# Kernel tuning notes

Hardware: AMD Instinct MI355X
Metric: run time of the kernel (lower is better)

## Reference

```python
import jax, jax.numpy as jnp
import numpy as np

B, N, Q, H = 32, 1024, 64, 768


def setup_inputs() -> dict:
    key = jax.random.key(0)
    k1, k2, k3, k4 = jax.random.split(key, 4)
    return {
        "nodes_compress": jax.random.normal(k1, (B, N, H), dtype=jnp.float32),
        "query_compress": jax.random.normal(k2, (B, Q, H), dtype=jnp.float32),
        "nodes_hidden": jax.random.normal(k3, (B, N, H), dtype=jnp.float32),
        # nn.Linear(3H, 1, bias=False).weight flattened to (3H,)
        "w": jax.random.normal(k4, (3 * H,), dtype=jnp.float32) * (1.0 / np.sqrt(3 * H)),
    }


def reference(nodes_compress, query_compress, nodes_hidden, w):
    h = nodes_compress.shape[-1]
    w_n, w_q, w_nq = w[:h], w[h:2 * h], w[2 * h:]
    # Decomposed trilinear similarity: identical to Linear([n, q, n*q]) -> scalar
    sim = (
        (nodes_compress @ w_n)[:, :, None]          # (B, N, 1)
        + (query_compress @ w_q)[:, None, :]        # (B, 1, Q)
        + jnp.einsum("bnh,bqh,h->bnq", nodes_compress, query_compress, w_nq)
    )                                                # (B, N, Q)
    # nodes -> query attention
    a = jax.nn.softmax(sim, axis=-1)                 # (B, N, Q)
    nodes2query = jnp.einsum("bnq,bqh->bnh", a, query_compress)
    # query -> nodes attention (max over query, softmax over nodes)
    b = jax.nn.softmax(jnp.max(sim, axis=-1), axis=-1)  # (B, N)
    q2n = jnp.einsum("bn,bnh->bh", b, nodes_compress)[:, None, :]  # (B, 1, H)
    q2n = jnp.broadcast_to(q2n, nodes_compress.shape)               # (B, N, H)
    return jnp.concatenate(
        [nodes_compress, nodes2query, nodes_compress * nodes2query, nodes_compress * q2n],
        axis=-1,
    )  # (B, N, 4H)
```

## Files before the change

### kernel.cpp

```cpp
#include <hip/hip_runtime.h>
#include <hip/hip_bf16.h>

#define BB 32
#define NN 1024
#define QQ 64
#define HH 768

typedef __attribute__((ext_vector_type(8))) short short8;
typedef __attribute__((ext_vector_type(4))) float f32x4;

#define GLOAD_LDS16(gp, lp) \
  __builtin_amdgcn_global_load_lds((const __attribute__((address_space(1))) unsigned int*)(gp), \
                                   (__attribute__((address_space(3))) unsigned int*)(lp), 16, 0, 0)

__device__ __forceinline__ unsigned short f2b(float f) {
  unsigned int u = __float_as_uint(f);
  unsigned int r = u + 0x7fffu + ((u >> 16) & 1u);
  return (unsigned short)(r >> 16);
}

__global__ void k_prep(const float* __restrict__ qc, const float* __restrict__ w,
                       unsigned short* __restrict__ qwB, unsigned short* __restrict__ qcT,
                       float* __restrict__ sq) {
  const int bid = blockIdx.x, tid = threadIdx.x;
  if (bid < 768) {
    int gid = bid * 256 + tid;
    int b = gid / 6144, rem = gid % 6144;
    int q = rem / 96, kk = rem % 96;
    int kc = kk >> 4, uu = kk & 15;
    const float* src = qc + ((size_t)(b * 64 + q) * HH + kk * 8);
    float4 g0 = *(const float4*)src, g1 = *(const float4*)(src + 4);
    int h = kk * 8;
    float4 n0 = *(const float4*)(w + h), n1 = *(const float4*)(w + h + 4);
    float4 m0 = *(const float4*)(w + 2 * HH + h), m1 = *(const float4*)(w + 2 * HH + h + 4);
    short8 v;
    v[0] = (short)f2b(g0.x * m0.x + n0.x); v[1] = (short)f2b(g0.y * m0.y + n0.y);
    v[2] = (short)f2b(g0.z * m0.z + n0.z); v[3] = (short)f2b(g0.w * m0.w + n0.w);
    v[4] = (short)f2b(g1.x * m1.x + n1.x); v[5] = (short)f2b(g1.y * m1.y + n1.y);
    v[6] = (short)f2b(g1.z * m1.z + n1.z); v[7] = (short)f2b(g1.w * m1.w + n1.w);
    size_t du = (size_t)(b * 6 + kc) * 1024 + q * 16 + (uu ^ (q & 7));
    *(short8*)((char*)qwB + du * 16) = v;
  } else if (bid < 1536) {
    int gid = (bid - 768) * 256 + tid;
    int b = gid / 6144, p = gid % 6144;
    int hc = p >> 10, pr = p & 1023, r = pr >> 3, x = pr & 7;
    int xu = x ^ (r & 7);
    int h = hc * 128 + r;
    const float* col = qc + ((size_t)(b * 64 + xu * 8) * HH + h);
    short8 v;
#pragma unroll
    for (int j = 0; j < 8; ++j) v[j] = (short)f2b(col[(size_t)j * HH]);
    *(short8*)((char*)qcT + (size_t)gid * 16) = v;
  } else {
    int wid = ((bid - 1536) * 256 + tid) >> 6;
    int l = tid & 63;
    const float* row = qc + (size_t)wid * HH;
    float s = 0.f;
#pragma unroll
    for (int i = 0; i < 12; ++i) s += row[i * 64 + l] * w[HH + i * 64 + l];
#pragma unroll
    for (int m = 1; m < 64; m <<= 1) s += __shfl_xor(s, m);
    if (l == 0) sq[wid] = s;
  }
}

__global__ __launch_bounds__(256) void k_sim(
    const float* __restrict__ nc, const unsigned short* __restrict__ qwB,
    const float* __restrict__ sq, float* __restrict__ partial,
    float* __restrict__ mtse, unsigned short* __restrict__ probs)
{
  __shared__ __align__(16) char bbuf[2][16384];
  __shared__ float rowmF[64];
  __shared__ float wvF[64];

  const int tid = threadIdx.x;
  const int wv_ = tid >> 6, l = tid & 63;
  const int l15 = l & 15, lg = l >> 4;
  const int b = blockIdx.x >> 4, tile = blockIdx.x & 15;
  const int row0 = tile * 64;

  const float* ncB = nc + (size_t)(b * NN + row0) * HH;
  const char* qwb = (const char*)qwB + (size_t)b * 98304;
  const float* aBase = ncB + (wv_ * 16 + l15) * HH + lg * 8;

  {
    const char* gsrc = qwb + wv_ * 4096 + l * 16;
#pragma unroll
    for (int i = 0; i < 4; ++i)
      GLOAD_LDS16(gsrc + i * 1024, &bbuf[0][wv_ * 4096 + i * 1024]);
  }
  float4 fr[2][8];
#pragma unroll
  for (int ks = 0; ks < 4; ++ks) {
    fr[0][ks * 2]     = *(const float4*)(aBase + ks * 32);
    fr[0][ks * 2 + 1] = *(const float4*)(aBase + ks * 32 + 4);
  }

  f32x4 acc[4] = {};
#pragma unroll
  for (int kc = 0; kc < 6; ++kc) {
    short8 af[4];
#pragma unroll
    for (int ks = 0; ks < 4; ++ks) {
      float4 f0 = fr[kc & 1][ks * 2], f1 = fr[kc & 1][ks * 2 + 1];
      short8 v;
      v[0] = (short)f2b(f0.x); v[1] = (short)f2b(f0.y);
      v[2] = (short)f2b(f0.z); v[3] = (short)f2b(f0.w);
      v[4] = (short)f2b(f1.x); v[5] = (short)f2b(f1.y);
      v[6] = (short)f2b(f1.z); v[7] = (short)f2b(f1.w);
      af[ks] = v;
    }
    if (kc < 5) {
#pragma unroll
      for (int ks = 0; ks < 4; ++ks) {
        fr[(kc + 1) & 1][ks * 2]     = *(const float4*)(aBase + (kc + 1) * 128 + ks * 32);
        fr[(kc + 1) & 1][ks * 2 + 1] = *(const float4*)(aBase + (kc + 1) * 128 + ks * 32 + 4);
      }
      const char* gsrc = qwb + (kc + 1) * 16384 + wv_ * 4096 + l * 16;
#pragma unroll
      for (int i = 0; i < 4; ++i)
        GLOAD_LDS16(gsrc + i * 1024, &bbuf[(kc + 1) & 1][wv_ * 4096 + i * 1024]);
      asm volatile("s_waitcnt vmcnt(12)" ::: "memory");
    } else {
      asm volatile("s_waitcnt vmcnt(0)" ::: "memory");
    }
    __builtin_amdgcn_s_barrier();
    __builtin_amdgcn_sched_barrier(0);
#pragma unroll
    for (int ks = 0; ks < 4; ++ks) {
      int kbyte = ks * 64 + lg * 16;
#pragma unroll
      for (int nt = 0; nt < 4; ++nt) {
        int brow = nt * 16 + l15;
        short8 bf = *(short8*)(&bbuf[kc & 1][0] + brow * 256 + (kbyte ^ ((l & 7) << 4)));
        acc[nt] = __builtin_amdgcn_mfma_f32_16x16x32_bf16(af[ks], bf, acc[nt], 0, 0, 0);
      }
    }
    __builtin_amdgcn_sched_barrier(0);
    __builtin_amdgcn_s_barrier();
  }

  unsigned short* pT = probs + (size_t)(b * 16 + tile) * (QQ * QQ);
  float sqv[4];
#pragma unroll
  for (int nt = 0; nt < 4; ++nt) sqv[nt] = sq[b * QQ + nt * 16 + l15];
#pragma unroll
  for (int j = 0; j < 4; ++j) {
    float mm = -1e30f;
#pragma unroll
    for (int nt = 0; nt < 4; ++nt) { acc[nt][j] += sqv[nt]; mm = fmaxf(mm, acc[nt][j]); }
    mm = fmaxf(mm, __shfl_xor(mm, 1));
    mm = fmaxf(mm, __shfl_xor(mm, 2));
    mm = fmaxf(mm, __shfl_xor(mm, 4));
    mm = fmaxf(mm, __shfl_xor(mm, 8));
    float ss = 0.f;
#pragma unroll
    for (int nt = 0; nt < 4; ++nt) { float p = __expf(acc[nt][j] - mm); acc[nt][j] = p; ss += p; }
    ss += __shfl_xor(ss, 1); ss += __shfl_xor(ss, 2);
    ss += __shfl_xor(ss, 4); ss += __shfl_xor(ss, 8);
    float inv = 1.0f / ss;
    int r = wv_ * 16 + lg * 4 + j;
#pragma unroll
    for (int nt = 0; nt < 4; ++nt)
      pT[r * 64 + nt * 16 + l15] = f2b(acc[nt][j] * inv);
    if (l15 == 0) rowmF[r] = mm;
  }
  __syncthreads();

  float m_t = -1e30f;
#pragma unroll
  for (int i = 0; i < 16; ++i) {
    f32x4 v = ((f32x4*)rowmF)[i];
    m_t = fmaxf(m_t, fmaxf(fmaxf(v[0], v[1]), fmaxf(v[2], v[3])));
  }
  if (tid < 64) wvF[tid] = __expf(rowmF[tid] - m_t);
  __syncthreads();
  {
    float sv = wvF[l];
#pragma unroll
    for (int m = 1; m < 64; m <<= 1) sv += __shfl_xor(sv, m);
    if (tid == 0) {
      mtse[(b * 16 + tile) * 2] = m_t;
      mtse[(b * 16 + tile) * 2 + 1] = sv;
    }
  }
  {
    float p0 = 0.f, p1 = 0.f, p2 = 0.f;
    for (int n = 0; n < 64; ++n) {
      float wvv = wvF[n];
      const float* pr = ncB + n * HH + tid;
      p0 += wvv * pr[0]; p1 += wvv * pr[256]; p2 += wvv * pr[512];
    }
    float* pp = partial + (size_t)(b * 16 + tile) * HH + tid;
    pp[0] = p0; pp[256] = p1; pp[512] = p2;
  }
}

__global__ __launch_bounds__(256) void k_out(
    const float* __restrict__ nc, const unsigned short* __restrict__ qcT,
    const unsigned short* __restrict__ probs, const float* __restrict__ partial,
    const float* __restrict__ mtse, float* __restrict__ out)
{
  __shared__ __align__(16) char smem[16384];
  __shared__ float q2nL[128];

  const int tid = threadIdx.x;
  const int wv_ = tid >> 6, l = tid & 63;
  const int l15 = l & 15, lg = l >> 4;
  const int bid = blockIdx.x;
  const int hc = bid % 6;
  const int bt = bid / 6;
  const int b = bt >> 4, tile = bt & 15;
  const int row0 = tile * 64;

  {
    const char* src = (const char*)qcT + ((size_t)(b * 6 + hc) << 14) + wv_ * 4096 + l * 16;
#pragma unroll
    for (int i = 0; i < 4; ++i)
      GLOAD_LDS16(src + i * 1024, &smem[wv_ * 4096 + i * 1024]);
  }

  if (tid < 128) {
    float M = -1e30f, mt[16], se[16];
#pragma unroll
    for (int i = 0; i < 16; ++i) {
      mt[i] = mtse[(b * 16 + i) * 2];
      se[i] = mtse[(b * 16 + i) * 2 + 1];
      M = fmaxf(M, mt[i]);
    }
    float denom = 0.f;
#pragma unroll
    for (int i = 0; i < 16; ++i) { mt[i] = __expf(mt[i] - M); denom += mt[i] * se[i]; }
    float inv = 1.0f / denom;
    float a = 0.f;
#pragma unroll
    for (int i = 0; i < 16; ++i)
      a += mt[i] * partial[(size_t)(b * 16 + i) * HH + hc * 128 + tid];
    q2nL[tid] = a * inv;
  }

  const unsigned short* pT = probs + (size_t)bt * (QQ * QQ);
  short8 a2_0 = *(const short8*)((const char*)pT + (wv_ * 16 + l15) * 128 + lg * 16);
  short8 a2_1 = *(const short8*)((const char*)pT + (wv_ * 16 + l15) * 128 + 64 + lg * 16);

  asm volatile("s_waitcnt vmcnt(0)" ::: "memory");
  __syncthreads();

  const int n = wv_ * 16 + l15;
  const float* ncrow = nc + (size_t)(b * NN + row0 + n) * HH;
  float* orow = out + (size_t)(b * NN + row0 + n) * 3072;

#pragma unroll
  for (int hg = 0; hg < 8; ++hg) {
    f32x4 c2 = {};
#pragma unroll
    for (int ks2 = 0; ks2 < 2; ++ks2) {
      int hrow = hg * 16 + l15;
      int kbyte = ks2 * 64 + lg * 16;
      short8 hf = *(short8*)(&smem[0] + hrow * 128 + (kbyte ^ ((l & 7) << 4)));
      c2 = __builtin_amdgcn_mfma_f32_16x16x32_bf16(hf, ks2 ? a2_1 : a2_0, c2, 0, 0, 0);
    }
    int hl = hg * 16 + lg * 4;
    int hbase = hc * 128 + hl;
    f32x4 ncv = *(const f32x4*)(ncrow + hbase);
    f32x4 qv  = *(const f32x4*)(&q2nL[hl]);
    *(f32x4*)(orow + hbase)          = ncv;
    *(f32x4*)(orow + HH + hbase)     = c2;
    *(f32x4*)(orow + 2 * HH + hbase) = ncv * c2;
    *(f32x4*)(orow + 2304 + hbase)   = ncv * qv;
  }
}

extern "C" void kernel_launch(void* const* d_in, const int* in_sizes, int n_in,
                              void* d_out, int out_size, void* d_ws, size_t ws_size,
                              hipStream_t stream) {
  (void)in_sizes; (void)n_in; (void)out_size; (void)ws_size;
  const float* nc = (const float*)d_in[0];
  const float* qc = (const float*)d_in[1];
  const float* w  = (const float*)d_in[3];
  float* out = (float*)d_out;
  char* ws = (char*)d_ws;
  unsigned short* qwB = (unsigned short*)(ws);
  unsigned short* qcT = (unsigned short*)(ws + 3145728);
  float* sqv     = (float*)(ws + 6291456);
  float* partial = (float*)(ws + 6299648);
  float* mtse    = (float*)(ws + 7872512);
  unsigned short* probs = (unsigned short*)(ws + 7876608);

  k_prep<<<2048, 256, 0, stream>>>(qc, w, qwB, qcT, sqv);
  k_sim<<<512, 256, 0, stream>>>(nc, qwB, sqv, partial, mtse, probs);
  k_out<<<3072, 256, 0, stream>>>(nc, qcT, probs, partial, mtse, out);
}
```

Before: 170.1 us.

## Fuse sim and output kernels via cooperative grid sync, keep probs in LDS

Merges the similarity/softmax kernel and the output kernel into one cooperative kernel of 512 blocks. A grid-wide sync separates the per-tile max/sum reduction from the q2n combine. The probability tile now stays in shared memory instead of a global round trip, and each block loops over all six H-chunks, double-buffering the transposed query chunks through registers into LDS. The cost is a grid barrier, fewer blocks to hide memory latency on the 400MB output write, and a dependence on every block being co-resident.

```diff
diff --git a/kernel.cpp b/kernel.cpp
--- a/kernel.cpp
+++ b/kernel.cpp
@@ -1,5 +1,8 @@
 #include <hip/hip_runtime.h>
 #include <hip/hip_bf16.h>
+#include <hip/hip_cooperative_groups.h>
+
+namespace cg = cooperative_groups;
 
 #define BB 32
 #define NN 1024
@@ -64,12 +67,15 @@
   }
 }
 
-__global__ __launch_bounds__(256) void k_sim(
+__global__ __launch_bounds__(256, 2) void k_fused(
     const float* __restrict__ nc, const unsigned short* __restrict__ qwB,
-    const float* __restrict__ sq, float* __restrict__ partial,
-    float* __restrict__ mtse, unsigned short* __restrict__ probs)
+    const unsigned short* __restrict__ qcT, const float* __restrict__ sq,
+    float* __restrict__ partial, float* __restrict__ mtse,
+    float* __restrict__ out)
 {
   __shared__ __align__(16) char bbuf[2][16384];
+  __shared__ __align__(16) char pbuf[8192];
+  __shared__ float q2nL[768];
   __shared__ float rowmF[64];
   __shared__ float wvF[64];
 
@@ -140,7 +146,6 @@
     __builtin_amdgcn_s_barrier();
   }
 
-  unsigned short* pT = probs + (size_t)(b * 16 + tile) * (QQ * QQ);
   float sqv[4];
 #pragma unroll
   for (int nt = 0; nt < 4; ++nt) sqv[nt] = sq[b * QQ + nt * 16 + l15];
@@ -162,7 +167,8 @@
     int r = wv_ * 16 + lg * 4 + j;
 #pragma unroll
     for (int nt = 0; nt < 4; ++nt)
-      pT[r * 64 + nt * 16 + l15] = f2b(acc[nt][j] * inv);
+      *(unsigned short*)(pbuf + r * 128 + ((nt * 32 + l15 * 2) ^ ((r & 7) << 4))) =
+          f2b(acc[nt][j] * inv);
     if (l15 == 0) rowmF[r] = mm;
   }
   __syncthreads();
@@ -194,33 +200,19 @@
     float* pp = partial + (size_t)(b * 16 + tile) * HH + tid;
     pp[0] = p0; pp[256] = p1; pp[512] = p2;
   }
-}
-
-__global__ __launch_bounds__(256) void k_out(
-    const float* __restrict__ nc, const unsigned short* __restrict__ qcT,
-    const unsigned short* __restrict__ probs, const float* __restrict__ partial,
-    const float* __restrict__ mtse, float* __restrict__ out)
-{
-  __shared__ __align__(16) char smem[16384];
-  __shared__ float q2nL[128];
-
-  const int tid = threadIdx.x;
-  const int wv_ = tid >> 6, l = tid & 63;
-  const int l15 = l & 15, lg = l >> 4;
-  const int bid = blockIdx.x;
-  const int hc = bid % 6;
-  const int bt = bid / 6;
-  const int b = bt >> 4, tile = bt & 15;
-  const int row0 = tile * 64;
-
-  {
-    const char* src = (const char*)qcT + ((size_t)(b * 6 + hc) << 14) + wv_ * 4096 + l * 16;
-#pragma unroll
-    for (int i = 0; i < 4; ++i)
-      GLOAD_LDS16(src + i * 1024, &smem[wv_ * 4096 + i * 1024]);
-  }
-
-  if (tid < 128) {
+
+  const int rr = wv_ * 16 + l15;
+  short8 a2_0 = *(short8*)(pbuf + rr * 128 + ((lg * 16) ^ ((rr & 7) << 4)));
+  short8 a2_1 = *(short8*)(pbuf + rr * 128 + ((64 + lg * 16) ^ ((rr & 7) << 4)));
+  const char* qcTb = (const char*)qcT + (size_t)(b * 6) * 16384 + wv_ * 4096 + l * 16;
+  short8 st[4];
+#pragma unroll
+  for (int i = 0; i < 4; ++i) st[i] = *(const short8*)(qcTb + i * 1024);
+
+  __threadfence();
+  cg::this_grid().sync();
+
+  {
     float M = -1e30f, mt[16], se[16];
 #pragma unroll
     for (int i = 0; i < 16; ++i) {
@@ -232,42 +224,50 @@
 #pragma unroll
     for (int i = 0; i < 16; ++i) { mt[i] = __expf(mt[i] - M); denom += mt[i] * se[i]; }
     float inv = 1.0f / denom;
-    float a = 0.f;
-#pragma unroll
-    for (int i = 0; i < 16; ++i)
-      a += mt[i] * partial[(size_t)(b * 16 + i) * HH + hc * 128 + tid];
-    q2nL[tid] = a * inv;
-  }
-
-  const unsigned short* pT = probs + (size_t)bt * (QQ * QQ);
-  short8 a2_0 = *(const short8*)((const char*)pT + (wv_ * 16 + l15) * 128 + lg * 16);
-  short8 a2_1 = *(const short8*)((const char*)pT + (wv_ * 16 + l15) * 128 + 64 + lg * 16);
-
-  asm volatile("s_waitcnt vmcnt(0)" ::: "memory");
+    float a0 = 0.f, a1 = 0.f, a2s = 0.f;
+#pragma unroll
+    for (int i = 0; i < 16; ++i) {
+      const float* pp = partial + (size_t)(b * 16 + i) * HH + tid;
+      float c = mt[i];
+      a0 += c * pp[0]; a1 += c * pp[256]; a2s += c * pp[512];
+    }
+    q2nL[tid] = a0 * inv; q2nL[tid + 256] = a1 * inv; q2nL[tid + 512] = a2s * inv;
+  }
   __syncthreads();
 
-  const int n = wv_ * 16 + l15;
-  const float* ncrow = nc + (size_t)(b * NN + row0 + n) * HH;
-  float* orow = out + (size_t)(b * NN + row0 + n) * 3072;
-
-#pragma unroll
-  for (int hg = 0; hg < 8; ++hg) {
-    f32x4 c2 = {};
-#pragma unroll
-    for (int ks2 = 0; ks2 < 2; ++ks2) {
-      int hrow = hg * 16 + l15;
-      int kbyte = ks2 * 64 + lg * 16;
-      short8 hf = *(short8*)(&smem[0] + hrow * 128 + (kbyte ^ ((l & 7) << 4)));
-      c2 = __builtin_amdgcn_mfma_f32_16x16x32_bf16(hf, ks2 ? a2_1 : a2_0, c2, 0, 0, 0);
-    }
-    int hl = hg * 16 + lg * 4;
-    int hbase = hc * 128 + hl;
-    f32x4 ncv = *(const f32x4*)(ncrow + hbase);
-    f32x4 qv  = *(const f32x4*)(&q2nL[hl]);
-    *(f32x4*)(orow + hbase)          = ncv;
-    *(f32x4*)(orow + HH + hbase)     = c2;
-    *(f32x4*)(orow + 2 * HH + hbase) = ncv * c2;
-    *(f32x4*)(orow + 2304 + hbase)   = ncv * qv;
+  const float* ncrow = nc + (size_t)(b * NN + row0 + rr) * HH;
+  float* orow = out + (size_t)(b * NN + row0 + rr) * 3072;
+
+  for (int hc = 0; hc < 6; ++hc) {
+    char* cur = bbuf[hc & 1];
+#pragma unroll
+    for (int i = 0; i < 4; ++i)
+      *(short8*)(cur + wv_ * 4096 + i * 1024 + l * 16) = st[i];
+    if (hc < 5) {
+#pragma unroll
+      for (int i = 0; i < 4; ++i)
+        st[i] = *(const short8*)(qcTb + (hc + 1) * 16384 + i * 1024);
+    }
+    __syncthreads();
+#pragma unroll
+    for (int hg = 0; hg < 8; ++hg) {
+      f32x4 c2 = {};
+#pragma unroll
+      for (int ks2 = 0; ks2 < 2; ++ks2) {
+        int hrow = hg * 16 + l15;
+        int kbyte = ks2 * 64 + lg * 16;
+        short8 hf = *(short8*)(cur + hrow * 128 + (kbyte ^ ((l & 7) << 4)));
+        c2 = __builtin_amdgcn_mfma_f32_16x16x32_bf16(hf, ks2 ? a2_1 : a2_0, c2, 0, 0, 0);
+      }
+      int hl = hg * 16 + lg * 4;
+      int hbase = hc * 128 + hl;
+      f32x4 ncv = *(const f32x4*)(ncrow + hbase);
+      f32x4 qv  = *(const f32x4*)(&q2nL[hbase]);
+      *(f32x4*)(orow + hbase)          = ncv;
+      *(f32x4*)(orow + HH + hbase)     = c2;
+      *(f32x4*)(orow + 2 * HH + hbase) = ncv * c2;
+      *(f32x4*)(orow + 2304 + hbase)   = ncv * qv;
+    }
   }
 }
 
@@ -285,9 +285,11 @@
   float* sqv     = (float*)(ws + 6291456);
   float* partial = (float*)(ws + 6299648);
   float* mtse    = (float*)(ws + 7872512);
-  unsigned short* probs = (unsigned short*)(ws + 7876608);
 
   k_prep<<<2048, 256, 0, stream>>>(qc, w, qwB, qcT, sqv);
-  k_sim<<<512, 256, 0, stream>>>(nc, qwB, sqv, partial, mtse, probs);
-  k_out<<<3072, 256, 0, stream>>>(nc, qcT, probs, partial, mtse, out);
-}
+
+  void* args[] = {(void*)&nc, (void*)&qwB, (void*)&qcT, (void*)&sqv,
+                  (void*)&partial, (void*)&mtse, (void*)&out};
+  hipLaunchCooperativeKernel((const void*)k_fused, dim3(512), dim3(256),
+                             args, 0, stream);
+}
```

Measured after the change: 301.9 us. +77.5%, slower.

## Split k_sim into 32-row tiles with query-column halves across waves

Applied to the files above, without the earlier changes.

k_sim now handles 32 node rows per block instead of 64, with the four waves split as two row groups by two query halves, and launches 1024 blocks instead of 512. Row softmax max and sum are combined across the two query halves through shared memory and extra barriers. k_out is updated to read the new probability tile layout and to reduce over 32 partials per batch. The aim is more parallelism and occupancy in the similarity kernel, at the cost of extra barriers, a second reduction pass, and each block loading the full B matrix while using only half of it per wave.

```diff
diff --git a/kernel.cpp b/kernel.cpp
--- a/kernel.cpp
+++ b/kernel.cpp
@@ -64,24 +64,26 @@
   }
 }
 
-__global__ __launch_bounds__(256) void k_sim(
+__global__ __launch_bounds__(256, 4) void k_sim(
     const float* __restrict__ nc, const unsigned short* __restrict__ qwB,
     const float* __restrict__ sq, float* __restrict__ partial,
     float* __restrict__ mtse, unsigned short* __restrict__ probs)
 {
   __shared__ __align__(16) char bbuf[2][16384];
-  __shared__ float rowmF[64];
-  __shared__ float wvF[64];
+  __shared__ float redM[2][32];
+  __shared__ float redS[2][32];
+  __shared__ float wvF[32];
 
   const int tid = threadIdx.x;
   const int wv_ = tid >> 6, l = tid & 63;
   const int l15 = l & 15, lg = l >> 4;
-  const int b = blockIdx.x >> 4, tile = blockIdx.x & 15;
-  const int row0 = tile * 64;
+  const int rg = wv_ & 1, qh = wv_ >> 1;
+  const int b = blockIdx.x >> 5, t32 = blockIdx.x & 31;
+  const int row0 = t32 * 32;
 
   const float* ncB = nc + (size_t)(b * NN + row0) * HH;
   const char* qwb = (const char*)qwB + (size_t)b * 98304;
-  const float* aBase = ncB + (wv_ * 16 + l15) * HH + lg * 8;
+  const float* aBase = ncB + (rg * 16 + l15) * HH + lg * 8;
 
   {
     const char* gsrc = qwb + wv_ * 4096 + l * 16;
@@ -96,7 +98,7 @@
     fr[0][ks * 2 + 1] = *(const float4*)(aBase + ks * 32 + 4);
   }
 
-  f32x4 acc[4] = {};
+  f32x4 acc[2] = {};
 #pragma unroll
   for (int kc = 0; kc < 6; ++kc) {
     short8 af[4];
@@ -130,8 +132,8 @@
     for (int ks = 0; ks < 4; ++ks) {
       int kbyte = ks * 64 + lg * 16;
 #pragma unroll
-      for (int nt = 0; nt < 4; ++nt) {
-        int brow = nt * 16 + l15;
+      for (int nt = 0; nt < 2; ++nt) {
+        int brow = qh * 32 + nt * 16 + l15;
         short8 bf = *(short8*)(&bbuf[kc & 1][0] + brow * 256 + (kbyte ^ ((l & 7) << 4)));
         acc[nt] = __builtin_amdgcn_mfma_f32_16x16x32_bf16(af[ks], bf, acc[nt], 0, 0, 0);
       }
@@ -140,58 +142,69 @@
     __builtin_amdgcn_s_barrier();
   }
 
-  unsigned short* pT = probs + (size_t)(b * 16 + tile) * (QQ * QQ);
-  float sqv[4];
-#pragma unroll
-  for (int nt = 0; nt < 4; ++nt) sqv[nt] = sq[b * QQ + nt * 16 + l15];
+  unsigned short* pT = probs + (size_t)(b * 32 + t32) * (32 * QQ);
+  float sqv[2];
+#pragma unroll
+  for (int nt = 0; nt < 2; ++nt) sqv[nt] = sq[b * QQ + qh * 32 + nt * 16 + l15];
+
 #pragma unroll
   for (int j = 0; j < 4; ++j) {
     float mm = -1e30f;
 #pragma unroll
-    for (int nt = 0; nt < 4; ++nt) { acc[nt][j] += sqv[nt]; mm = fmaxf(mm, acc[nt][j]); }
+    for (int nt = 0; nt < 2; ++nt) { acc[nt][j] += sqv[nt]; mm = fmaxf(mm, acc[nt][j]); }
     mm = fmaxf(mm, __shfl_xor(mm, 1));
     mm = fmaxf(mm, __shfl_xor(mm, 2));
     mm = fmaxf(mm, __shfl_xor(mm, 4));
     mm = fmaxf(mm, __shfl_xor(mm, 8));
+    if (l15 == 0) redM[qh][rg * 16 + lg * 4 + j] = mm;
+  }
+  __syncthreads();
+#pragma unroll
+  for (int j = 0; j < 4; ++j) {
+    int r = rg * 16 + lg * 4 + j;
+    float mm = fmaxf(redM[0][r], redM[1][r]);
     float ss = 0.f;
 #pragma unroll
-    for (int nt = 0; nt < 4; ++nt) { float p = __expf(acc[nt][j] - mm); acc[nt][j] = p; ss += p; }
+    for (int nt = 0; nt < 2; ++nt) { float p = __expf(acc[nt][j] - mm); acc[nt][j] = p; ss += p; }
     ss += __shfl_xor(ss, 1); ss += __shfl_xor(ss, 2);
     ss += __shfl_xor(ss, 4); ss += __shfl_xor(ss, 8);
-    float inv = 1.0f / ss;
-    int r = wv_ * 16 + lg * 4 + j;
-#pragma unroll
-    for (int nt = 0; nt < 4; ++nt)
-      pT[r * 64 + nt * 16 + l15] = f2b(acc[nt][j] * inv);
-    if (l15 == 0) rowmF[r] = mm;
+    if (l15 == 0) redS[qh][r] = ss;
   }
   __syncthreads();
+#pragma unroll
+  for (int j = 0; j < 4; ++j) {
+    int r = rg * 16 + lg * 4 + j;
+    float inv = 1.0f / (redS[0][r] + redS[1][r]);
+#pragma unroll
+    for (int nt = 0; nt < 2; ++nt)
+      pT[r * 64 + qh * 32 + nt * 16 + l15] = f2b(acc[nt][j] * inv);
+  }
 
   float m_t = -1e30f;
 #pragma unroll
   for (int i = 0; i < 16; ++i) {
-    f32x4 v = ((f32x4*)rowmF)[i];
+    f32x4 v = ((f32x4*)&redM[0][0])[i];
     m_t = fmaxf(m_t, fmaxf(fmaxf(v[0], v[1]), fmaxf(v[2], v[3])));
   }
-  if (tid < 64) wvF[tid] = __expf(rowmF[tid] - m_t);
+  if (tid < 32) wvF[tid] = __expf(fmaxf(redM[0][tid], redM[1][tid]) - m_t);
   __syncthreads();
   {
-    float sv = wvF[l];
+    float sv = (l < 32) ? wvF[l] : 0.f;
 #pragma unroll
     for (int m = 1; m < 64; m <<= 1) sv += __shfl_xor(sv, m);
     if (tid == 0) {
-      mtse[(b * 16 + tile) * 2] = m_t;
-      mtse[(b * 16 + tile) * 2 + 1] = sv;
+      mtse[(b * 32 + t32) * 2] = m_t;
+      mtse[(b * 32 + t32) * 2 + 1] = sv;
     }
   }
   {
     float p0 = 0.f, p1 = 0.f, p2 = 0.f;
-    for (int n = 0; n < 64; ++n) {
+    for (int n = 0; n < 32; ++n) {
       float wvv = wvF[n];
       const float* pr = ncB + n * HH + tid;
       p0 += wvv * pr[0]; p1 += wvv * pr[256]; p2 += wvv * pr[512];
     }
-    float* pp = partial + (size_t)(b * 16 + tile) * HH + tid;
+    float* pp = partial + (size_t)(b * 32 + t32) * HH + tid;
     pp[0] = p0; pp[256] = p1; pp[512] = p2;
   }
 }
@@ -221,34 +234,33 @@
   }
 
   if (tid < 128) {
-    float M = -1e30f, mt[16], se[16];
-#pragma unroll
-    for (int i = 0; i < 16; ++i) {
-      mt[i] = mtse[(b * 16 + i) * 2];
-      se[i] = mtse[(b * 16 + i) * 2 + 1];
-      M = fmaxf(M, mt[i]);
-    }
+    float M = -1e30f;
+#pragma unroll
+    for (int i = 0; i < 32; ++i) M = fmaxf(M, mtse[(b * 32 + i) * 2]);
     float denom = 0.f;
 #pragma unroll
-    for (int i = 0; i < 16; ++i) { mt[i] = __expf(mt[i] - M); denom += mt[i] * se[i]; }
+    for (int i = 0; i < 32; ++i)
+      denom += __expf(mtse[(b * 32 + i) * 2] - M) * mtse[(b * 32 + i) * 2 + 1];
     float inv = 1.0f / denom;
     float a = 0.f;
 #pragma unroll
-    for (int i = 0; i < 16; ++i)
-      a += mt[i] * partial[(size_t)(b * 16 + i) * HH + hc * 128 + tid];
+    for (int i = 0; i < 32; ++i)
+      a += __expf(mtse[(b * 32 + i) * 2] - M) *
+           partial[(size_t)(b * 32 + i) * HH + hc * 128 + tid];
     q2nL[tid] = a * inv;
   }
 
-  const unsigned short* pT = probs + (size_t)bt * (QQ * QQ);
-  short8 a2_0 = *(const short8*)((const char*)pT + (wv_ * 16 + l15) * 128 + lg * 16);
-  short8 a2_1 = *(const short8*)((const char*)pT + (wv_ * 16 + l15) * 128 + 64 + lg * 16);
+  const int rr = wv_ * 16 + l15;
+  const int t32 = tile * 2 + (rr >> 5), pr = rr & 31;
+  const unsigned short* pT = probs + (size_t)(b * 32 + t32) * (32 * QQ);
+  short8 a2_0 = *(const short8*)((const char*)pT + pr * 128 + lg * 16);
+  short8 a2_1 = *(const short8*)((const char*)pT + pr * 128 + 64 + lg * 16);
 
   asm volatile("s_waitcnt vmcnt(0)" ::: "memory");
   __syncthreads();
 
-  const int n = wv_ * 16 + l15;
-  const float* ncrow = nc + (size_t)(b * NN + row0 + n) * HH;
-  float* orow = out + (size_t)(b * NN + row0 + n) * 3072;
+  const float* ncrow = nc + (size_t)(b * NN + row0 + rr) * HH;
+  float* orow = out + (size_t)(b * NN + row0 + rr) * 3072;
 
 #pragma unroll
   for (int hg = 0; hg < 8; ++hg) {
@@ -284,10 +296,10 @@
   unsigned short* qcT = (unsigned short*)(ws + 3145728);
   float* sqv     = (float*)(ws + 6291456);
   float* partial = (float*)(ws + 6299648);
-  float* mtse    = (float*)(ws + 7872512);
-  unsigned short* probs = (unsigned short*)(ws + 7876608);
+  float* mtse    = (float*)(ws + 9445376);
+  unsigned short* probs = (unsigned short*)(ws + 9453568);
 
   k_prep<<<2048, 256, 0, stream>>>(qc, w, qwB, qcT, sqv);
-  k_sim<<<512, 256, 0, stream>>>(nc, qwB, sqv, partial, mtse, probs);
+  k_sim<<<1024, 256, 0, stream>>>(nc, qwB, sqv, partial, mtse, probs);
   k_out<<<3072, 256, 0, stream>>>(nc, qcT, probs, partial, mtse, out);
 }
```

Result: slower. 178.8 us (+5.1%).

## Read B operand directly from global memory instead of staging through LDS

Applied to the files above, without the earlier changes.

The qwB prep now writes a plain row-major bf16 layout instead of a swizzled chunked layout. The sim kernel drops the double-buffered LDS staging, the manual register prefetch of A, the explicit waitcnt and the barriers. Each wave now loads A and B fragments straight from global memory (B through L2/L1) inside the MFMA loop. This removes LDS traffic and block-level synchronisation, but it loses the explicit overlap of loads with compute and the sharing of B across the four waves.

```diff
diff --git a/kernel.cpp b/kernel.cpp
--- a/kernel.cpp
+++ b/kernel.cpp
@@ -17,6 +17,15 @@
   unsigned int u = __float_as_uint(f);
   unsigned int r = u + 0x7fffu + ((u >> 16) & 1u);
   return (unsigned short)(r >> 16);
+}
+
+__device__ __forceinline__ short8 cvt8(float4 f0, float4 f1) {
+  short8 v;
+  v[0] = (short)f2b(f0.x); v[1] = (short)f2b(f0.y);
+  v[2] = (short)f2b(f0.z); v[3] = (short)f2b(f0.w);
+  v[4] = (short)f2b(f1.x); v[5] = (short)f2b(f1.y);
+  v[6] = (short)f2b(f1.z); v[7] = (short)f2b(f1.w);
+  return v;
 }
 
 __global__ void k_prep(const float* __restrict__ qc, const float* __restrict__ w,
@@ -25,12 +34,9 @@
   const int bid = blockIdx.x, tid = threadIdx.x;
   if (bid < 768) {
     int gid = bid * 256 + tid;
-    int b = gid / 6144, rem = gid % 6144;
-    int q = rem / 96, kk = rem % 96;
-    int kc = kk >> 4, uu = kk & 15;
-    const float* src = qc + ((size_t)(b * 64 + q) * HH + kk * 8);
+    int h = (gid * 8) % HH;
+    const float* src = qc + (size_t)gid * 8;
     float4 g0 = *(const float4*)src, g1 = *(const float4*)(src + 4);
-    int h = kk * 8;
     float4 n0 = *(const float4*)(w + h), n1 = *(const float4*)(w + h + 4);
     float4 m0 = *(const float4*)(w + 2 * HH + h), m1 = *(const float4*)(w + 2 * HH + h + 4);
     short8 v;
@@ -38,8 +44,7 @@
     v[2] = (short)f2b(g0.z * m0.z + n0.z); v[3] = (short)f2b(g0.w * m0.w + n0.w);
     v[4] = (short)f2b(g1.x * m1.x + n1.x); v[5] = (short)f2b(g1.y * m1.y + n1.y);
     v[6] = (short)f2b(g1.z * m1.z + n1.z); v[7] = (short)f2b(g1.w * m1.w + n1.w);
-    size_t du = (size_t)(b * 6 + kc) * 1024 + q * 16 + (uu ^ (q & 7));
-    *(short8*)((char*)qwB + du * 16) = v;
+    *(short8*)(qwB + (size_t)gid * 8) = v;
   } else if (bid < 1536) {
     int gid = (bid - 768) * 256 + tid;
     int b = gid / 6144, p = gid % 6144;
@@ -69,7 +74,6 @@
     const float* __restrict__ sq, float* __restrict__ partial,
     float* __restrict__ mtse, unsigned short* __restrict__ probs)
 {
-  __shared__ __align__(16) char bbuf[2][16384];
   __shared__ float rowmF[64];
   __shared__ float wvF[64];
 
@@ -80,64 +84,25 @@
   const int row0 = tile * 64;
 
   const float* ncB = nc + (size_t)(b * NN + row0) * HH;
-  const char* qwb = (const char*)qwB + (size_t)b * 98304;
-  const float* aBase = ncB + (wv_ * 16 + l15) * HH + lg * 8;
-
-  {
-    const char* gsrc = qwb + wv_ * 4096 + l * 16;
-#pragma unroll
-    for (int i = 0; i < 4; ++i)
-      GLOAD_LDS16(gsrc + i * 1024, &bbuf[0][wv_ * 4096 + i * 1024]);
-  }
-  float4 fr[2][8];
-#pragma unroll
-  for (int ks = 0; ks < 4; ++ks) {
-    fr[0][ks * 2]     = *(const float4*)(aBase + ks * 32);
-    fr[0][ks * 2 + 1] = *(const float4*)(aBase + ks * 32 + 4);
-  }
+  const int arow = wv_ * 16 + l15;
+  const float* aRow = ncB + (size_t)arow * HH + lg * 8;
+  const unsigned short* bRow = qwB + (size_t)b * QQ * HH + (size_t)l15 * HH + lg * 8;
 
   f32x4 acc[4] = {};
 #pragma unroll
   for (int kc = 0; kc < 6; ++kc) {
-    short8 af[4];
 #pragma unroll
     for (int ks = 0; ks < 4; ++ks) {
-      float4 f0 = fr[kc & 1][ks * 2], f1 = fr[kc & 1][ks * 2 + 1];
-      short8 v;
-      v[0] = (short)f2b(f0.x); v[1] = (short)f2b(f0.y);
-      v[2] = (short)f2b(f0.z); v[3] = (short)f2b(f0.w);
-      v[4] = (short)f2b(f1.x); v[5] = (short)f2b(f1.y);
-      v[6] = (short)f2b(f1.z); v[7] = (short)f2b(f1.w);
-      af[ks] = v;
-    }
-    if (kc < 5) {
-#pragma unroll
-      for (int ks = 0; ks < 4; ++ks) {
-        fr[(kc + 1) & 1][ks * 2]     = *(const float4*)(aBase + (kc + 1) * 128 + ks * 32);
-        fr[(kc + 1) & 1][ks * 2 + 1] = *(const float4*)(aBase + (kc + 1) * 128 + ks * 32 + 4);
+      int col = kc * 128 + ks * 32;
+      float4 f0 = *(const float4*)(aRow + col);
+      float4 f1 = *(const float4*)(aRow + col + 4);
+      short8 a = cvt8(f0, f1);
+#pragma unroll
+      for (int nt = 0; nt < 4; ++nt) {
+        short8 bf = *(const short8*)(bRow + nt * 16 * HH + col);
+        acc[nt] = __builtin_amdgcn_mfma_f32_16x16x32_bf16(a, bf, acc[nt], 0, 0, 0);
       }
-      const char* gsrc = qwb + (kc + 1) * 16384 + wv_ * 4096 + l * 16;
-#pragma unroll
-      for (int i = 0; i < 4; ++i)
-        GLOAD_LDS16(gsrc + i * 1024, &bbuf[(kc + 1) & 1][wv_ * 4096 + i * 1024]);
-      asm volatile("s_waitcnt vmcnt(12)" ::: "memory");
-    } else {
-      asm volatile("s_waitcnt vmcnt(0)" ::: "memory");
-    }
-    __builtin_amdgcn_s_barrier();
-    __builtin_amdgcn_sched_barrier(0);
-#pragma unroll
-    for (int ks = 0; ks < 4; ++ks) {
-      int kbyte = ks * 64 + lg * 16;
-#pragma unroll
-      for (int nt = 0; nt < 4; ++nt) {
-        int brow = nt * 16 + l15;
-        short8 bf = *(short8*)(&bbuf[kc & 1][0] + brow * 256 + (kbyte ^ ((l & 7) << 4)));
-        acc[nt] = __builtin_amdgcn_mfma_f32_16x16x32_bf16(af[ks], bf, acc[nt], 0, 0, 0);
-      }
-    }
-    __builtin_amdgcn_sched_barrier(0);
-    __builtin_amdgcn_s_barrier();
+    }
   }
 
   unsigned short* pT = probs + (size_t)(b * 16 + tile) * (QQ * QQ);
```

Measured after the change: 184.5 us. +8.4%, slower.
